# Kernel tuning notes

Measured on AMD Instinct MI355X. Metric: run time of the kernel, lower is better.

The kernel has to match this reference:

```python
import jax, jax.numpy as jnp
import numpy as np

B, N = 1, 1024
VOCAB = 32000
DIM = 512
DEPTH = 2
HEADS = 8
DIM_HEAD = 64
DIM_INNER = HEADS * DIM_HEAD      # 512
DIM_FF = 4 * DIM                  # 2048
MAX_SEQ = 1024
EPS = 1e-12


def sq_dist(x, w):
    # squared L2 distance between rows of x [..., d] and rows of w [m, d] -> [..., m]
    xs = jnp.sum(x * x, axis=-1, keepdims=True)
    ws = jnp.sum(w * w, axis=-1)
    return xs - 2.0 * jnp.einsum('...d,md->...m', x, w) + ws


def cdist(x, w):
    # euclidean distance (torch.cdist equivalent)
    return jnp.sqrt(jnp.maximum(sq_dist(x, w), 0.0))


def rmsnorm(x, gamma):
    # F.normalize(x, dim=-1) * sqrt(dim) * (gamma + 1)
    n = jnp.linalg.norm(x, axis=-1, keepdims=True)
    return x / jnp.maximum(n, EPS) * (DIM ** 0.5) * (gamma + 1.0)


def attention(x, qkv_w, out_w):
    b, n, _ = x.shape
    qkv = cdist(x, qkv_w)                                   # [b, n, 3*inner] (to_qkv: squared=False)
    qkv = qkv.reshape(b, n, 3, HEADS, DIM_HEAD)
    qkv = qkv.transpose(2, 0, 3, 1, 4)                      # [3, b, h, n, d]
    q, k, v = qkv[0], qkv[1], qkv[2]
    qs = jnp.sum(q * q, axis=-1)                            # [b, h, n]
    ks = jnp.sum(k * k, axis=-1)                            # [b, h, n]
    # -||q_i - k_j||^2 = 2 q.k - ||q||^2 - ||k||^2
    sim = (2.0 * jnp.einsum('bhid,bhjd->bhij', q, k)
           - qs[..., :, None] - ks[..., None, :]) * (DIM_HEAD ** -0.5)
    attn = jax.nn.softmax(sim, axis=-1)
    o = jnp.einsum('bhij,bhjd->bhid', attn, v)
    o = o.transpose(0, 2, 1, 3).reshape(b, n, DIM_INNER)    # merge heads
    return o @ out_w.T                                      # plain Linear, no bias


def feedforward(x, w_in, b_in, w_out):
    h = -sq_dist(x, w_in) + b_in                            # proj_in: squared=True, negate=True, bias
    h = jax.nn.gelu(h, approximate=False)
    return h @ w_out.T                                      # plain Linear, no bias


def setup_inputs() -> dict:
    key = jax.random.key(0)
    ks = jax.random.split(key, 12)
    nrm = lambda k, s: jax.random.normal(k, s, dtype=jnp.float32)
    return {
        'tokens': jax.random.randint(ks[0], (B, N), 0, VOCAB),
        'token_emb': nrm(ks[1], (VOCAB, DIM)),
        'pos_emb': nrm(ks[2], (MAX_SEQ, DIM)),
        'qkv_w': nrm(ks[3], (DEPTH, 3 * DIM_INNER, DIM)),
        'attn_out_w': nrm(ks[4], (DEPTH, DIM, DIM_INNER)) * 0.02,
        'ff_in_w': nrm(ks[5], (DEPTH, DIM_FF, DIM)),
        'ff_in_b': nrm(ks[6], (DEPTH, DIM_FF)),
        'ff_out_w': nrm(ks[7], (DEPTH, DIM, DIM_FF)) * 0.02,
        'attn_gamma': jnp.zeros((DEPTH, DIM), jnp.float32),
        'ff_gamma': jnp.zeros((DEPTH, DIM), jnp.float32),
        'final_gamma': jnp.zeros((DIM,), jnp.float32),
    }


def reference(tokens, token_emb, pos_emb, qkv_w, attn_out_w, ff_in_w, ff_in_b,
              ff_out_w, attn_gamma, ff_gamma, final_gamma):
    n = tokens.shape[-1]
    x = token_emb[tokens] + pos_emb[:n]                     # [b, n, dim]
    for l in range(DEPTH):
        x = attention(rmsnorm(x, attn_gamma[l]), qkv_w[l], attn_out_w[l]) + x
        x = feedforward(rmsnorm(x, ff_gamma[l]), ff_in_w[l], ff_in_b[l], ff_out_w[l]) + x
    x = rmsnorm(x, final_gamma)
    return -sq_dist(x, token_emb)                           # [b, n, vocab] logits
```

## Files before the change

kernel.cpp:

```cpp
#include <hip/hip_runtime.h>
#include <math.h>

#define DIMM  512
#define NSEQ  1024
#define NHEAD 8
#define DH    64
#define DFF   2048
#define NVOC  32000
#define NDEPTH 2
#define VCENTER 32.0f
#define KVB   64
#define QBLK  32
#define QKOFF ((size_t)NHEAD * NSEQ * DH)

typedef __attribute__((ext_vector_type(8))) __bf16 bf16x8;
typedef __attribute__((ext_vector_type(4))) float f32x4;

__device__ __forceinline__ void g2l16(const void* g, void* l) {
    __builtin_amdgcn_global_load_lds(
        (const __attribute__((address_space(1))) void*)g,
        (__attribute__((address_space(3))) void*)l, 16, 0, 0);
}

#define WAITV(N) asm volatile("s_waitcnt vmcnt(" #N ")" ::: "memory")

__launch_bounds__(256)
__global__ void embed_rms(const int* __restrict__ tokens,
                          const float* __restrict__ temb,
                          const float* __restrict__ pemb,
                          const float* __restrict__ gamma,
                          float* __restrict__ x,
                          __bf16* __restrict__ y, float* __restrict__ xs) {
    int i = blockIdx.x;
    int tid = threadIdx.x;
    int tok = tokens[i];
    const float* e = temb + (size_t)tok * DIMM;
    const float* p = pemb + (size_t)i * DIMM;
    float v0 = e[tid] + p[tid];
    float v1 = e[tid + 256] + p[tid + 256];
    x[(size_t)i * DIMM + tid]       = v0;
    x[(size_t)i * DIMM + tid + 256] = v1;
    float ss = v0 * v0 + v1 * v1;
    __shared__ float red[4];
    #pragma unroll
    for (int off = 32; off; off >>= 1) ss += __shfl_down(ss, off, 64);
    if ((tid & 63) == 0) red[tid >> 6] = ss;
    __syncthreads();
    float tot = red[0] + red[1] + red[2] + red[3];
    float scale = 22.627416997969522f / fmaxf(sqrtf(tot), 1e-12f);
    float y0 = v0 * scale * (gamma[tid] + 1.0f);
    float y1 = v1 * scale * (gamma[tid + 256] + 1.0f);
    y[(size_t)i * DIMM + tid]       = (__bf16)y0;
    y[(size_t)i * DIMM + tid + 256] = (__bf16)y1;
    float s2 = y0 * y0 + y1 * y1;
    __syncthreads();
    #pragma unroll
    for (int off = 32; off; off >>= 1) s2 += __shfl_down(s2, off, 64);
    if ((tid & 63) == 0) red[tid >> 6] = s2;
    __syncthreads();
    if (tid == 0) xs[i] = red[0] + red[1] + red[2] + red[3];
}

template<int S>
__launch_bounds__(256)
__global__ void rms_red(const float* __restrict__ parts, float* __restrict__ x,
                        const float* __restrict__ gamma,
                        __bf16* __restrict__ y, float* __restrict__ xs) {
    int i = blockIdx.x;
    int tid = threadIdx.x;
    float* xr = x + (size_t)i * DIMM;
    float v0 = xr[tid], v1 = xr[tid + 256];
    #pragma unroll
    for (int s = 0; s < S; s++) {
        const float* pr = parts + (size_t)s * NSEQ * DIMM + (size_t)i * DIMM;
        v0 += pr[tid];
        v1 += pr[tid + 256];
    }
    xr[tid] = v0;
    xr[tid + 256] = v1;
    float ss = v0 * v0 + v1 * v1;
    __shared__ float red[4];
    #pragma unroll
    for (int off = 32; off; off >>= 1) ss += __shfl_down(ss, off, 64);
    if ((tid & 63) == 0) red[tid >> 6] = ss;
    __syncthreads();
    float tot = red[0] + red[1] + red[2] + red[3];
    float scale = 22.627416997969522f / fmaxf(sqrtf(tot), 1e-12f);
    float y0 = v0 * scale * (gamma[tid] + 1.0f);
    float y1 = v1 * scale * (gamma[tid + 256] + 1.0f);
    y[(size_t)i * DIMM + tid]       = (__bf16)y0;
    y[(size_t)i * DIMM + tid + 256] = (__bf16)y1;
    float s2 = y0 * y0 + y1 * y1;
    __syncthreads();
    #pragma unroll
    for (int off = 32; off; off >>= 1) s2 += __shfl_down(s2, off, 64);
    if ((tid & 63) == 0) red[tid >> 6] = s2;
    __syncthreads();
    if (tid == 0) xs[i] = red[0] + red[1] + red[2] + red[3];
}

__launch_bounds__(256)
__global__ void conv_all(const float* __restrict__ qkv_w, const float* __restrict__ attn_out_w,
                         const float* __restrict__ ff_in_w, const float* __restrict__ ff_out_w,
                         const float* __restrict__ temb,
                         __bf16* __restrict__ wq16, __bf16* __restrict__ wa16,
                         __bf16* __restrict__ wfi16, __bf16* __restrict__ wfo16,
                         __bf16* __restrict__ temb16,
                         float* __restrict__ wsq_qkv, float* __restrict__ wsq_ff,
                         float* __restrict__ wsq_temb) {
    int bid = blockIdx.x;
    const float* src; __bf16* dst; float* ssq; int K = DIMM;
    if (bid < NDEPTH * 3 * DIMM) {
        src = qkv_w;  dst = wq16;  ssq = wsq_qkv;
    } else if ((bid -= NDEPTH * 3 * DIMM) < NDEPTH * DIMM) {
        src = attn_out_w; dst = wa16; ssq = nullptr;
    } else if ((bid -= NDEPTH * DIMM) < NDEPTH * DFF) {
        src = ff_in_w; dst = wfi16; ssq = wsq_ff;
    } else if ((bid -= NDEPTH * DFF) < NDEPTH * DIMM) {
        src = ff_out_w; dst = wfo16; ssq = nullptr; K = DFF;
    } else {
        bid -= NDEPTH * DIMM;
        src = temb; dst = temb16; ssq = wsq_temb;
    }
    const float* s = src + (size_t)bid * K;
    __bf16* d = dst + (size_t)bid * K;
    float ss = 0.f;
    for (int j = threadIdx.x; j < K; j += 256) {
        float v = s[j];
        d[j] = (__bf16)v;
        ss += v * v;
    }
    __shared__ float red[4];
    #pragma unroll
    for (int off = 32; off; off >>= 1) ss += __shfl_down(ss, off, 64);
    if ((threadIdx.x & 63) == 0) red[threadIdx.x >> 6] = ss;
    __syncthreads();
    if (threadIdx.x == 0 && ssq) ssq[bid] = red[0] + red[1] + red[2] + red[3];
}

enum { MODE_LINEAR = 0, MODE_CDIST = 1, MODE_FFGELU = 2, MODE_LOGITS = 3 };

template<int MODE>
__device__ __forceinline__ void write_elem(void* Cout, int r, int c, int M, float dot,
                                           float xsr, const float* __restrict__ ws,
                                           const float* __restrict__ bias) {
    if (MODE == MODE_LINEAR) {
        ((float*)Cout)[(size_t)r * M + c] = dot;
    } else if (MODE == MODE_FFGELU) {
        float d2 = xsr + ws[c] - 2.0f * dot;
        float hh = -d2 + bias[c];
        float v = 0.5f * hh * (1.0f + erff(hh * 0.70710678118654752f));
        ((__bf16*)Cout)[(size_t)r * M + c] = (__bf16)v;
    }
}

__launch_bounds__(512)
__global__ void gemm_logits(const __bf16* __restrict__ A, const __bf16* __restrict__ W,
                            const float* __restrict__ xs, const float* __restrict__ ws,
                            float* __restrict__ out) {
    __shared__ __align__(16) __bf16 As[6 * 128 * 32];
    __shared__ __align__(16) __bf16 Bs[6 * 256 * 32];
    const int tid = threadIdx.x;
    const int lane = tid & 63;
    const int wv = tid >> 6;
    const int wr = wv >> 2, wc = wv & 3;

    int id = blockIdx.x;
    id = (id & 7) * 125 + (id >> 3);
    const int row0 = (id & 7) * 128;
    const int col0 = (id >> 3) * 256;

    const int scol = ((tid & 3) ^ ((tid >> 3) & 3)) * 8;
    const __bf16* gA = A + (size_t)(row0 + (tid >> 2)) * DIMM + scol;
    const __bf16* gB = W + (size_t)(col0 + (tid >> 2)) * DIMM + scol;
    const int lrow = lane & 15;
    const int l4 = lane >> 4;
    const int slot = (l4 ^ ((lrow >> 1) & 3)) * 8;

    auto stageChunk = [&](int k0, int b) {
        g2l16(gA + k0,                      &As[b * 4096 + tid * 8]);
        g2l16(gB + k0,                      &Bs[b * 8192 + tid * 8]);
        g2l16(gB + (size_t)128 * DIMM + k0, &Bs[b * 8192 + 4096 + tid * 8]);
    };

    f32x4 acc[4][4] = {};
    const int nP = DIMM >> 6;
    stageChunk(0, 0);  stageChunk(32, 1);
    stageChunk(64, 2); stageChunk(96, 3);
    int pb = 0;
    for (int p = 0; p < nP; p++) {
        if (p < nP - 1) WAITV(6); else WAITV(0);
        __builtin_amdgcn_s_barrier();
        __builtin_amdgcn_sched_barrier(0);
        if (p + 2 < nP) {
            int nb = pb + 2; if (nb >= 3) nb -= 3;
            stageChunk((p + 2) << 6,        nb * 2);
            stageChunk(((p + 2) << 6) + 32, nb * 2 + 1);
        }
        #pragma unroll
        for (int half = 0; half < 2; half++) {
            const int b = pb * 2 + half;
            bf16x8 af[4], bfr[4];
            #pragma unroll
            for (int m = 0; m < 4; m++)
                af[m] = *(const bf16x8*)&As[b * 4096 + (wr * 64 + m * 16 + lrow) * 32 + slot];
            #pragma unroll
            for (int n = 0; n < 4; n++)
                bfr[n] = *(const bf16x8*)&Bs[b * 8192 + (wc * 64 + n * 16 + lrow) * 32 + slot];
            #pragma unroll
            for (int m = 0; m < 4; m++)
                #pragma unroll
                for (int n = 0; n < 4; n++)
                    acc[m][n] = __builtin_amdgcn_mfma_f32_16x16x32_bf16(af[m], bfr[n], acc[m][n], 0, 0, 0);
        }
        if (++pb == 3) pb = 0;
    }

    const int r_base = row0 + wr * 64 + l4 * 4;
    const int c_base = col0 + wc * 64 + lrow;
    #pragma unroll
    for (int m = 0; m < 4; m++)
        #pragma unroll
        for (int j = 0; j < 4; j++) {
            const int r = r_base + m * 16 + j;
            const float xsr = xs[r];
            #pragma unroll
            for (int n = 0; n < 4; n++) {
                const int c = c_base + n * 16;
                out[(size_t)r * NVOC + c] = -(xsr + ws[c] - 2.0f * acc[m][n][j]);
            }
        }
}

template<int MODE>
__launch_bounds__(256)
__global__ void gemm64(const __bf16* __restrict__ A, const __bf16* __restrict__ W,
                       const float* __restrict__ xs, const float* __restrict__ ws,
                       const float* __restrict__ bias,
                       void* __restrict__ Cout, int K, int Kstr, int M,
                       float* __restrict__ ksout) {
    __shared__ __align__(16) __bf16 As[6 * 64 * 32];
    __shared__ __align__(16) __bf16 Bs[6 * 64 * 32];
    __shared__ float ksred[2][64];
    const int tid = threadIdx.x;
    const int lane = tid & 63;
    const int wv = tid >> 6;
    const int wr = wv >> 1, wc = wv & 1;

    const int gx = gridDim.x;
    const int total = gx * gridDim.y;
    int id = blockIdx.y * gx + blockIdx.x;
    id = (id & 7) * (total >> 3) + (id >> 3);
    const int bx = id % gx;
    const int by = id / gx;
    const int row0 = by * 64;
    const int col0 = bx * 64;
    const size_t zoff = (size_t)blockIdx.z * K;
    float* Cz = (float*)Cout + (size_t)blockIdx.z * NSEQ * M;

    const int scol = (((tid & 3) ^ ((tid >> 3) & 3))) * 8;
    const __bf16* gA = A + (size_t)(row0 + (tid >> 2)) * Kstr + scol + zoff;
    const __bf16* gB = W + (size_t)(col0 + (tid >> 2)) * Kstr + scol + zoff;
    const int lrow = lane & 15;
    const int l4 = lane >> 4;
    const int slot = (l4 ^ ((lrow >> 1) & 3)) * 8;

    auto stageChunk = [&](int k0, int b) {
        g2l16(gA + k0, &As[b * 2048 + tid * 8]);
        g2l16(gB + k0, &Bs[b * 2048 + tid * 8]);
    };

    f32x4 acc[2][2] = {};
    const int nP = K >> 6;
    stageChunk(0, 0);  stageChunk(32, 1);
    stageChunk(64, 2); stageChunk(96, 3);
    int pb = 0;
    for (int p = 0; p < nP; p++) {
        if (p < nP - 1) WAITV(4); else WAITV(0);
        __builtin_amdgcn_s_barrier();
        __builtin_amdgcn_sched_barrier(0);
        if (p + 2 < nP) {
            int nb = pb + 2; if (nb >= 3) nb -= 3;
            stageChunk((p + 2) << 6,        nb * 2);
            stageChunk(((p + 2) << 6) + 32, nb * 2 + 1);
        }
        #pragma unroll
        for (int half = 0; half < 2; half++) {
            const int b = pb * 2 + half;
            bf16x8 af[2], bfr[2];
            #pragma unroll
            for (int m = 0; m < 2; m++)
                af[m] = *(const bf16x8*)&As[b * 2048 + (wr * 32 + m * 16 + lrow) * 32 + slot];
            #pragma unroll
            for (int n = 0; n < 2; n++)
                bfr[n] = *(const bf16x8*)&Bs[b * 2048 + (wc * 32 + n * 16 + lrow) * 32 + slot];
            #pragma unroll
            for (int m = 0; m < 2; m++)
                #pragma unroll
                for (int n = 0; n < 2; n++)
                    acc[m][n] = __builtin_amdgcn_mfma_f32_16x16x32_bf16(af[m], bfr[n], acc[m][n], 0, 0, 0);
        }
        if (++pb == 3) pb = 0;
    }

    const int r_base = row0 + wr * 32 + (lane >> 4) * 4;
    const int c_base = col0 + wc * 32 + (lane & 15);

    if (MODE == MODE_CDIST) {
        const int sec = col0 >> 9;
        const int h = (col0 >> 6) & 7;
        __bf16* Qc = (__bf16*)Cout;
        float pk[2][4];
        #pragma unroll
        for (int m = 0; m < 2; m++)
            #pragma unroll
            for (int j = 0; j < 4; j++) {
                const int r = r_base + m * 16 + j;
                const float xsr = xs[r];
                pk[m][j] = 0.f;
                #pragma unroll
                for (int n = 0; n < 2; n++) {
                    const int c = c_base + n * 16;
                    float d2 = xsr + ws[c] - 2.0f * acc[m][n][j];
                    float v = sqrtf(fmaxf(d2, 0.0f)) - VCENTER;
                    __bf16 bv = (__bf16)v;
                    const int d = c & 63;
                    if (sec == 0)      Qc[((size_t)h * NSEQ + r) * DH + d] = bv;
                    else if (sec == 1) Qc[QKOFF + ((size_t)h * NSEQ + r) * DH + d] = bv;
                    else               Qc[2 * QKOFF + ((size_t)h * DH + d) * NSEQ + r] = bv;
                    float fv = (float)bv;
                    pk[m][j] += fv * fv;
                }
            }
        if (sec == 1) {
            #pragma unroll
            for (int m = 0; m < 2; m++)
                #pragma unroll
                for (int j = 0; j < 4; j++) {
                    float v = pk[m][j];
                    #pragma unroll
                    for (int off = 1; off < 16; off <<= 1) v += __shfl_xor(v, off, 64);
                    if (lrow == 0) ksred[wc][wr * 32 + m * 16 + l4 * 4 + j] = v;
                }
            __syncthreads();
            if (tid < 64)
                ksout[(size_t)h * NSEQ + row0 + tid] = ksred[0][tid] + ksred[1][tid];
        }
    } else {
        #pragma unroll
        for (int m = 0; m < 2; m++)
            #pragma unroll
            for (int j = 0; j < 4; j++) {
                const int r = r_base + m * 16 + j;
                const float xsr = (MODE == MODE_LINEAR) ? 0.f : xs[r];
                #pragma unroll
                for (int n = 0; n < 2; n++)
                    write_elem<MODE>(Cz, r, c_base + n * 16, M, acc[m][n][j], xsr, ws, bias);
            }
    }
}

__launch_bounds__(128)
__global__ void flash_attn(const __bf16* __restrict__ Qc, const __bf16* __restrict__ Kc,
                           const __bf16* __restrict__ VcT, const float* __restrict__ ks,
                           __bf16* __restrict__ O) {
    __shared__ __align__(16) __bf16 Qs[QBLK * 64];
    __shared__ __align__(16) __bf16 Ks[2][64 * 64];
    __shared__ __align__(16) __bf16 Vs[2][64 * 64];
    __shared__ __align__(16) __bf16 Ps[2][16 * 64];
    __shared__ float kss[2][64];
    const int tid = threadIdx.x, lane = tid & 63, wv = tid >> 6;
    const int h = blockIdx.y, q0 = blockIdx.x * QBLK;
    const int l15 = lane & 15, l4 = lane >> 4;

    #pragma unroll
    for (int pass = 0; pass < 2; pass++) {
        int gl = tid + pass * 128, r = gl >> 3, gs = (gl & 7) ^ (r & 7);
        g2l16(Qc + ((size_t)h * NSEQ + q0 + r) * DH + gs * 8, &Qs[gl * 8]);
    }
    auto stage = [&](int c, int buf) {
        const int kv0 = c * KVB;
        #pragma unroll
        for (int pass = 0; pass < 4; pass++) {
            int gl = tid + pass * 128, r = gl >> 3, gs = (gl & 7) ^ (r & 7);
            g2l16(Kc + ((size_t)h * NSEQ + kv0 + r) * DH + gs * 8, &Ks[buf][gl * 8]);
            g2l16(VcT + ((size_t)h * DH + r) * NSEQ + kv0 + gs * 8, &Vs[buf][gl * 8]);
        }
        if (tid < KVB) kss[buf][tid] = ks[(size_t)h * NSEQ + c * KVB + tid];
    };
    stage(0, 0);
    __syncthreads();

    bf16x8 qf[2];
    #pragma unroll
    for (int s = 0; s < 2; s++) {
        int row = wv * 16 + l15;
        int g = (l4 + 4 * s) ^ (row & 7);
        qf[s] = *(const bf16x8*)&Qs[row * 64 + g * 8];
    }

    float m_j[4], l_j[4];
    f32x4 o_[4] = {};
    #pragma unroll
    for (int j = 0; j < 4; j++) { m_j[j] = -1e30f; l_j[j] = 0.f; }

    for (int c = 0; c < NSEQ / KVB; c++) {
        const int b = c & 1;
        if (c + 1 < NSEQ / KVB) stage(c + 1, b ^ 1);

        f32x4 sa[4] = {};
        #pragma unroll
        for (int s = 0; s < 2; s++) {
            bf16x8 kf[4];
            #pragma unroll
            for (int n = 0; n < 4; n++) {
                int row = n * 16 + l15;
                int g = (l4 + 4 * s) ^ (row & 7);
                kf[n] = *(const bf16x8*)&Ks[b][row * 64 + g * 8];
            }
            #pragma unroll
            for (int n = 0; n < 4; n++)
                sa[n] = __builtin_amdgcn_mfma_f32_16x16x32_bf16(qf[s], kf[n], sa[n], 0, 0, 0);
        }
        float ksv[4];
        #pragma unroll
        for (int n = 0; n < 4; n++) ksv[n] = kss[b][n * 16 + l15];

        float scale[4];
        #pragma unroll
        for (int j = 0; j < 4; j++) {
            float mx = -1e30f;
            #pragma unroll
            for (int n = 0; n < 4; n++) {
                float sv = sa[n][j] * 0.25f - ksv[n] * 0.125f;
                sa[n][j] = sv;
                mx = fmaxf(mx, sv);
            }
            #pragma unroll
            for (int off = 1; off < 16; off <<= 1) mx = fmaxf(mx, __shfl_xor(mx, off, 64));
            float mn = fmaxf(m_j[j], mx);
            scale[j] = expf(m_j[j] - mn);
            m_j[j] = mn;
        }
        #pragma unroll
        for (int j = 0; j < 4; j++) {
            const int row = l4 * 4 + j;
            float ls = 0.f;
            #pragma unroll
            for (int n = 0; n < 4; n++) {
                float pv = expf(sa[n][j] - m_j[j]);
                ls += pv;
                int col = n * 16 + l15;
                Ps[wv][row * 64 + ((((col >> 3) ^ (row & 7)) << 3) | (col & 7))] = (__bf16)pv;
            }
            #pragma unroll
            for (int off = 1; off < 16; off <<= 1) ls += __shfl_xor(ls, off, 64);
            l_j[j] = l_j[j] * scale[j] + ls;
            o_[0][j] *= scale[j]; o_[1][j] *= scale[j];
            o_[2][j] *= scale[j]; o_[3][j] *= scale[j];
        }

        #pragma unroll
        for (int s = 0; s < 2; s++) {
            int g = (l4 + 4 * s) ^ (l15 & 7);
            bf16x8 pf = *(const bf16x8*)&Ps[wv][l15 * 64 + g * 8];
            #pragma unroll
            for (int n = 0; n < 4; n++) {
                int row = n * 16 + l15;
                int gv = (l4 + 4 * s) ^ (row & 7);
                bf16x8 vf = *(const bf16x8*)&Vs[b][row * 64 + gv * 8];
                o_[n] = __builtin_amdgcn_mfma_f32_16x16x32_bf16(pf, vf, o_[n], 0, 0, 0);
            }
        }
        __syncthreads();
    }

    #pragma unroll
    for (int n = 0; n < 4; n++)
        #pragma unroll
        for (int j = 0; j < 4; j++) {
            int row = q0 + wv * 16 + l4 * 4 + j;
            int d = n * 16 + l15;
            O[(size_t)row * DIMM + h * DH + d] = (__bf16)(o_[n][j] / l_j[j] + VCENTER);
        }
}

extern "C" void kernel_launch(void* const* d_in, const int* in_sizes, int n_in,
                              void* d_out, int out_size, void* d_ws, size_t ws_size,
                              hipStream_t stream) {
    (void)in_sizes; (void)n_in; (void)out_size; (void)ws_size;
    const int*   tokens      = (const int*)d_in[0];
    const float* temb        = (const float*)d_in[1];
    const float* pemb        = (const float*)d_in[2];
    const float* qkv_w       = (const float*)d_in[3];
    const float* attn_out_w  = (const float*)d_in[4];
    const float* ff_in_w     = (const float*)d_in[5];
    const float* ff_in_b     = (const float*)d_in[6];
    const float* ff_out_w    = (const float*)d_in[7];
    const float* attn_gamma  = (const float*)d_in[8];
    const float* ff_gamma    = (const float*)d_in[9];
    const float* final_gamma = (const float*)d_in[10];
    float* out = (float*)d_out;

    char* p = (char*)d_ws;
    float*  x        = (float*)p;  p += (size_t)NSEQ * DIMM * 4;
    float*  xs       = (float*)p;  p += (size_t)NSEQ * 4;
    float*  wsq_qkv  = (float*)p;  p += (size_t)NDEPTH * 3 * DIMM * 4;
    float*  wsq_ff   = (float*)p;  p += (size_t)NDEPTH * DFF * 4;
    float*  wsq_temb = (float*)p;  p += (size_t)NVOC * 4;
    float*  ksbuf    = (float*)p;  p += (size_t)NHEAD * NSEQ * 4;
    float*  parts    = (float*)p;  p += (size_t)4 * NSEQ * DIMM * 4;
    __bf16* y16      = (__bf16*)p; p += (size_t)NSEQ * DIMM * 2;
    __bf16* o16      = (__bf16*)p; p += (size_t)NSEQ * DIMM * 2;
    __bf16* Qc       = (__bf16*)p; p += 3 * QKOFF * 2;
    __bf16* hb16     = (__bf16*)p; p += (size_t)NSEQ * DFF * 2;
    __bf16* wq16     = (__bf16*)p; p += (size_t)NDEPTH * 3 * DIMM * DIMM * 2;
    __bf16* wa16     = (__bf16*)p; p += (size_t)NDEPTH * DIMM * DIMM * 2;
    __bf16* wfi16    = (__bf16*)p; p += (size_t)NDEPTH * DFF * DIMM * 2;
    __bf16* wfo16    = (__bf16*)p; p += (size_t)NDEPTH * DIMM * DFF * 2;
    __bf16* temb16   = (__bf16*)p; p += (size_t)NVOC * DIMM * 2;
    __bf16* Kc  = Qc + QKOFF;
    __bf16* VcT = Qc + 2 * QKOFF;

    const int convBlocks = NDEPTH * 3 * DIMM + NDEPTH * DIMM + NDEPTH * DFF
                         + NDEPTH * DIMM + NVOC;
    conv_all<<<convBlocks, 256, 0, stream>>>(qkv_w, attn_out_w, ff_in_w, ff_out_w, temb,
                                             wq16, wa16, wfi16, wfo16, temb16,
                                             wsq_qkv, wsq_ff, wsq_temb);

    embed_rms<<<NSEQ, 256, 0, stream>>>(tokens, temb, pemb, attn_gamma, x, y16, xs);

    for (int l = 0; l < NDEPTH; l++) {
        const __bf16* qkvw = wq16  + (size_t)l * 3 * DIMM * DIMM;
        const __bf16* aow  = wa16  + (size_t)l * DIMM * DIMM;
        const __bf16* fiw  = wfi16 + (size_t)l * DFF * DIMM;
        const __bf16* fow  = wfo16 + (size_t)l * DIMM * DFF;
        const float*  fib  = ff_in_b + (size_t)l * DFF;
        const float*  next_gamma = (l + 1 < NDEPTH) ? (attn_gamma + (l + 1) * DIMM)
                                                    : final_gamma;

        gemm64<MODE_CDIST><<<dim3(3 * DIMM / 64, NSEQ / 64), 256, 0, stream>>>(
            y16, qkvw, xs, wsq_qkv + l * 3 * DIMM, nullptr, Qc, DIMM, DIMM, 3 * DIMM, ksbuf);
        flash_attn<<<dim3(NSEQ / QBLK, NHEAD), 128, 0, stream>>>(Qc, Kc, VcT, ksbuf, o16);
        gemm64<MODE_LINEAR><<<dim3(DIMM / 64, NSEQ / 64, 2), 256, 0, stream>>>(
            o16, aow, nullptr, nullptr, nullptr, parts, DIMM / 2, DIMM, DIMM, nullptr);
        rms_red<2><<<NSEQ, 256, 0, stream>>>(parts, x, ff_gamma + l * DIMM, y16, xs);

        gemm64<MODE_FFGELU><<<dim3(DFF / 64, NSEQ / 64), 256, 0, stream>>>(
            y16, fiw, xs, wsq_ff + l * DFF, fib, hb16, DIMM, DIMM, DFF, nullptr);
        gemm64<MODE_LINEAR><<<dim3(DIMM / 64, NSEQ / 64, 4), 256, 0, stream>>>(
            hb16, fow, nullptr, nullptr, nullptr, parts, DFF / 4, DFF, DIMM, nullptr);
        rms_red<4><<<NSEQ, 256, 0, stream>>>(parts, x, next_gamma, y16, xs);
    }

    gemm_logits<<<1000, 512, 0, stream>>>(y16, temb16, xs, wsq_temb, out);
}
```

Measured before the change: 252.4 us.

## Overlap token-embedding bf16 conversion with flash attention via extra blocks

The fp32-to-bf16 conversion and squared-norm computation of the 32000-row token embedding moves out of the upfront conversion kernel. It now runs as extra blocks appended to each layer's flash attention launch, half the vocabulary per layer. The aim is to fill idle compute units during attention, which launches only 256 blocks, so the bandwidth-heavy conversion no longer sits on the critical path. The cost is that attention blocks may now compete with the conversion for memory bandwidth, and the flash grid becomes one-dimensional with the head index derived from blockIdx.

```diff
diff --git a/kernel.cpp b/kernel.cpp
--- a/kernel.cpp
+++ b/kernel.cpp
@@ -12,8 +12,12 @@
 #define KVB   64
 #define QBLK  32
 #define QKOFF ((size_t)NHEAD * NSEQ * DH)
+#define FLASH_BLOCKS (NSEQ / QBLK * NHEAD)
+#define CONV_ROWS_PER_LAYER (NVOC / NDEPTH)
+#define CONV_BLOCKS (CONV_ROWS_PER_LAYER / 64)
 
 typedef __attribute__((ext_vector_type(8))) __bf16 bf16x8;
+typedef __attribute__((ext_vector_type(4))) __bf16 bf16x4;
 typedef __attribute__((ext_vector_type(4))) float f32x4;
 
 __device__ __forceinline__ void g2l16(const void* g, void* l) {
@@ -102,12 +106,9 @@
 __launch_bounds__(256)
 __global__ void conv_all(const float* __restrict__ qkv_w, const float* __restrict__ attn_out_w,
                          const float* __restrict__ ff_in_w, const float* __restrict__ ff_out_w,
-                         const float* __restrict__ temb,
                          __bf16* __restrict__ wq16, __bf16* __restrict__ wa16,
                          __bf16* __restrict__ wfi16, __bf16* __restrict__ wfo16,
-                         __bf16* __restrict__ temb16,
-                         float* __restrict__ wsq_qkv, float* __restrict__ wsq_ff,
-                         float* __restrict__ wsq_temb) {
+                         float* __restrict__ wsq_qkv, float* __restrict__ wsq_ff) {
     int bid = blockIdx.x;
     const float* src; __bf16* dst; float* ssq; int K = DIMM;
     if (bid < NDEPTH * 3 * DIMM) {
@@ -116,11 +117,9 @@
         src = attn_out_w; dst = wa16; ssq = nullptr;
     } else if ((bid -= NDEPTH * DIMM) < NDEPTH * DFF) {
         src = ff_in_w; dst = wfi16; ssq = wsq_ff;
-    } else if ((bid -= NDEPTH * DFF) < NDEPTH * DIMM) {
+    } else {
+        bid -= NDEPTH * DFF;
         src = ff_out_w; dst = wfo16; ssq = nullptr; K = DFF;
-    } else {
-        bid -= NDEPTH * DIMM;
-        src = temb; dst = temb16; ssq = wsq_temb;
     }
     const float* s = src + (size_t)bid * K;
     __bf16* d = dst + (size_t)bid * K;
@@ -363,14 +362,38 @@
 __launch_bounds__(128)
 __global__ void flash_attn(const __bf16* __restrict__ Qc, const __bf16* __restrict__ Kc,
                            const __bf16* __restrict__ VcT, const float* __restrict__ ks,
-                           __bf16* __restrict__ O) {
+                           __bf16* __restrict__ O,
+                           const float* __restrict__ temb, __bf16* __restrict__ temb16,
+                           float* __restrict__ wsq_temb, int conv_row0) {
+    const int tid = threadIdx.x, lane = tid & 63, wv = tid >> 6;
+
+    if (blockIdx.x >= FLASH_BLOCKS) {
+        const int base = conv_row0 + (blockIdx.x - FLASH_BLOCKS) * 64;
+        for (int it = 0; it < 32; it++) {
+            const int row = base + it * 2 + wv;
+            const float* src = temb + (size_t)row * DIMM;
+            float4 a = ((const float4*)src)[lane];
+            float4 b2 = ((const float4*)src)[lane + 64];
+            float ss = a.x * a.x + a.y * a.y + a.z * a.z + a.w * a.w
+                     + b2.x * b2.x + b2.y * b2.y + b2.z * b2.z + b2.w * b2.w;
+            bf16x4 oa, ob;
+            oa.x = (__bf16)a.x;  oa.y = (__bf16)a.y;  oa.z = (__bf16)a.z;  oa.w = (__bf16)a.w;
+            ob.x = (__bf16)b2.x; ob.y = (__bf16)b2.y; ob.z = (__bf16)b2.z; ob.w = (__bf16)b2.w;
+            *(bf16x4*)&temb16[(size_t)row * DIMM + lane * 4]       = oa;
+            *(bf16x4*)&temb16[(size_t)row * DIMM + 256 + lane * 4] = ob;
+            #pragma unroll
+            for (int off = 32; off; off >>= 1) ss += __shfl_down(ss, off, 64);
+            if (lane == 0) wsq_temb[row] = ss;
+        }
+        return;
+    }
+
     __shared__ __align__(16) __bf16 Qs[QBLK * 64];
     __shared__ __align__(16) __bf16 Ks[2][64 * 64];
     __shared__ __align__(16) __bf16 Vs[2][64 * 64];
     __shared__ __align__(16) __bf16 Ps[2][16 * 64];
     __shared__ float kss[2][64];
-    const int tid = threadIdx.x, lane = tid & 63, wv = tid >> 6;
-    const int h = blockIdx.y, q0 = blockIdx.x * QBLK;
+    const int h = blockIdx.x >> 5, q0 = (blockIdx.x & 31) * QBLK;
     const int l15 = lane & 15, l4 = lane >> 4;
 
     #pragma unroll
@@ -523,10 +546,10 @@
     __bf16* VcT = Qc + 2 * QKOFF;
 
     const int convBlocks = NDEPTH * 3 * DIMM + NDEPTH * DIMM + NDEPTH * DFF
-                         + NDEPTH * DIMM + NVOC;
-    conv_all<<<convBlocks, 256, 0, stream>>>(qkv_w, attn_out_w, ff_in_w, ff_out_w, temb,
-                                             wq16, wa16, wfi16, wfo16, temb16,
-                                             wsq_qkv, wsq_ff, wsq_temb);
+                         + NDEPTH * DIMM;
+    conv_all<<<convBlocks, 256, 0, stream>>>(qkv_w, attn_out_w, ff_in_w, ff_out_w,
+                                             wq16, wa16, wfi16, wfo16,
+                                             wsq_qkv, wsq_ff);
 
     embed_rms<<<NSEQ, 256, 0, stream>>>(tokens, temb, pemb, attn_gamma, x, y16, xs);
 
@@ -541,7 +564,8 @@
 
         gemm64<MODE_CDIST><<<dim3(3 * DIMM / 64, NSEQ / 64), 256, 0, stream>>>(
             y16, qkvw, xs, wsq_qkv + l * 3 * DIMM, nullptr, Qc, DIMM, DIMM, 3 * DIMM, ksbuf);
-        flash_attn<<<dim3(NSEQ / QBLK, NHEAD), 128, 0, stream>>>(Qc, Kc, VcT, ksbuf, o16);
+        flash_attn<<<FLASH_BLOCKS + CONV_BLOCKS, 128, 0, stream>>>(
+            Qc, Kc, VcT, ksbuf, o16, temb, temb16, wsq_temb, l * CONV_ROWS_PER_LAYER);
         gemm64<MODE_LINEAR><<<dim3(DIMM / 64, NSEQ / 64, 2), 256, 0, stream>>>(
             o16, aow, nullptr, nullptr, nullptr, parts, DIMM / 2, DIMM, DIMM, nullptr);
         rms_red<2><<<NSEQ, 256, 0, stream>>>(parts, x, ff_gamma + l * DIMM, y16, xs);
```

New measurement: 232.2 us. -8.0%, faster.
